# Kernel optimization log

Measured on AMD Instinct MI355X. Metric: run time of the kernel, lower is better.

Reference implementation:

```python
import jax, jax.numpy as jnp
import numpy as np

LN_EPS = 1e-3  # Keras LayerNormalization default epsilon


def setup_inputs() -> dict:
    key = jax.random.key(0)
    ks = jax.random.split(key, 6)
    B, H, W, C = 8, 64, 64, 256
    s = 1.0 / np.sqrt(C)
    return {
        "x": jax.random.normal(ks[0], (B, H, W, C), dtype=jnp.float32),
        "ln_gamma": jnp.ones((C,), jnp.float32),
        "ln_beta": jnp.zeros((C,), jnp.float32),
        "w_q": jax.random.normal(ks[1], (C, C), jnp.float32) * s,
        "b_q": jnp.zeros((C,), jnp.float32),
        "w_k": jax.random.normal(ks[2], (C, C), jnp.float32) * s,
        "b_k": jnp.zeros((C,), jnp.float32),
        "w_v": jax.random.normal(ks[3], (C, C), jnp.float32) * s,
        "b_v": jnp.zeros((C,), jnp.float32),
        "w_p": jax.random.normal(ks[4], (C, C), jnp.float32) * s,
        "b_p": jnp.zeros((C,), jnp.float32),
    }


def reference(x, ln_gamma, ln_beta, w_q, b_q, w_k, b_k, w_v, b_v, w_p, b_p):
    B, H, W, C = x.shape
    units = w_q.shape[1]
    scale = jnp.asarray(units, x.dtype) ** (-0.5)

    # LayerNormalization over the channel axis (Keras default eps=1e-3)
    mean = jnp.mean(x, axis=-1, keepdims=True)
    var = jnp.mean(jnp.square(x - mean), axis=-1, keepdims=True)
    xn = (x - mean) * jax.lax.rsqrt(var + LN_EPS) * ln_gamma + ln_beta

    xf = xn.reshape(B, H * W, C)  # flatten spatial grid to N tokens
    q = xf @ w_q + b_q
    k = xf @ w_k + b_k
    v = xf @ w_v + b_v

    # full quadratic attention over N = H*W tokens
    scores = jnp.einsum("bnc,bmc->bnm", q, k) * scale  # [B, N, N]
    attn = jax.nn.softmax(scores, axis=-1)
    out = jnp.einsum("bnm,bmc->bnc", attn, v)  # [B, N, units]
    proj = (out @ w_p + b_p).reshape(B, H, W, units)

    # NOTE: original code reassigns inputs = norm(inputs), so the residual
    # uses the normalized input, not the raw input.
    return xn + proj
```

## Files before the change

kernel.cpp:

```cpp
#include <hip/hip_runtime.h>
#include <cstdint>

#define NB    8
#define NSEQ  4096
#define CDIM  256
#define NTOK  (NB*NSEQ)

typedef _Float16 half8  __attribute__((ext_vector_type(8)));
typedef _Float16 half4v __attribute__((ext_vector_type(4)));
typedef float    f32x4  __attribute__((ext_vector_type(4)));
typedef float    f32x16 __attribute__((ext_vector_type(16)));
typedef uint32_t u32x4  __attribute__((ext_vector_type(4)));
typedef unsigned long u64x2 __attribute__((ext_vector_type(2)));

typedef unsigned int u32_g __attribute__((address_space(1)));
typedef unsigned int u32_l __attribute__((address_space(3)));

__device__ __forceinline__ void gload_lds16(const void* g, void* l) {
  __builtin_amdgcn_global_load_lds((u32_g*)(uintptr_t)g,
                                   (u32_l*)(uint32_t)(uintptr_t)l, 16, 0, 0);
}

__device__ __forceinline__ uint32_t pkrtz(float a, float b) {
  auto h = __builtin_amdgcn_cvt_pkrtz(a, b);
  return __builtin_bit_cast(uint32_t, h);
}
__device__ __forceinline__ uint8_t to_fp8(float v) {
  return (uint8_t)(__builtin_amdgcn_cvt_pk_fp8_f32(v, v, 0, false) & 0xff);
}
__device__ __forceinline__ float sx32f(float v) { return __shfl_xor(v, 32, 64); }
__device__ __forceinline__ uint32_t sx32u(uint32_t v) {
  return (uint32_t)__shfl_xor((int)v, 32, 64);
}

__global__ __launch_bounds__(256) void ln_kernel(
    const float* __restrict__ x, const float* __restrict__ gam,
    const float* __restrict__ bet, _Float16* __restrict__ xnh) {
  const int lane = threadIdx.x & 63;
  const size_t tok = (size_t)blockIdx.x * 4 + (threadIdx.x >> 6);
  const float4 v = ((const float4*)(x + tok * CDIM))[lane];
  float s  = v.x + v.y + v.z + v.w;
  float s2 = v.x*v.x + v.y*v.y + v.z*v.z + v.w*v.w;
  #pragma unroll
  for (int m = 1; m < 64; m <<= 1) {
    s  += __shfl_xor(s,  m, 64);
    s2 += __shfl_xor(s2, m, 64);
  }
  const float mean = s * (1.0f / CDIM);
  const float rstd = rsqrtf(s2 * (1.0f / CDIM) - mean * mean + 1e-3f);
  const float4 gv = ((const float4*)gam)[lane];
  const float4 bv = ((const float4*)bet)[lane];
  half4v h;
  h[0] = (_Float16)((v.x - mean) * rstd * gv.x + bv.x);
  h[1] = (_Float16)((v.y - mean) * rstd * gv.y + bv.y);
  h[2] = (_Float16)((v.z - mean) * rstd * gv.z + bv.z);
  h[3] = (_Float16)((v.w - mean) * rstd * gv.w + bv.w);
  ((half4v*)(xnh + tok * CDIM))[lane] = h;
}

__global__ __launch_bounds__(256, 2) void proj_kernel(
    const _Float16* __restrict__ inh,
    const float* __restrict__ wq_, const float* __restrict__ bq_,
    const float* __restrict__ wk_, const float* __restrict__ bk_,
    const float* __restrict__ wv_, const float* __restrict__ bv_,
    const float* __restrict__ wp_, const float* __restrict__ bp_,
    uint8_t* __restrict__ qg8, uint8_t* __restrict__ kg8,
    _Float16* __restrict__ vtg,
    const _Float16* __restrict__ residh, float* __restrict__ outf,
    int mode_base) {
  extern __shared__ char smem[];
  const int mode = mode_base + blockIdx.z;
  const float* wsel = (mode == 0) ? wq_ : (mode == 1) ? wk_ : (mode == 2) ? wv_ : wp_;
  const float* bsel = (mode == 0) ? bq_ : (mode == 1) ? bk_ : (mode == 2) ? bv_ : bp_;

  const int tid = threadIdx.x;
  const int lane = tid & 63;
  const int wid  = tid >> 6;
  const int g    = lane >> 4;
  const int lr   = lane & 15;
  const int jstrip = blockIdx.y;
  const size_t tok0 = (size_t)blockIdx.x * 512;

  char* wt   = smem;
  char* tile = smem + 32768;

  for (int i = 0; i < 64; ++i) {
    int idx = i * 256 + tid;
    int c = idx >> 6, j = idx & 63;
    float val = wsel[(size_t)c * CDIM + jstrip * 64 + j];
    *(_Float16*)(wt + j * 512 + ((((c >> 3) ^ (j & 7))) << 4) + ((c & 7) << 1)) =
        (_Float16)val;
  }
  float bjv[4];
  #pragma unroll
  for (int jc = 0; jc < 4; ++jc) bjv[jc] = bsel[jstrip * 64 + jc * 16 + lr];
  __syncthreads();

  for (int t = 0; t < 8; ++t) {
    const size_t trow0 = tok0 + t * 64;
    #pragma unroll
    for (int i = 0; i < 8; ++i) {
      int pbase = (i * 4 + wid) * 64;
      int p = pbase + lane;
      int row = p >> 5, sl = p & 31;
      gload_lds16(inh + (trow0 + row) * CDIM + (size_t)((sl ^ (row & 7)) * 8),
                  tile + pbase * 16);
    }
    __syncthreads();

    f32x4 acc[4] = {{0,0,0,0},{0,0,0,0},{0,0,0,0},{0,0,0,0}};
    #pragma unroll
    for (int kc = 0; kc < 8; ++kc) {
      half8 a = *(const half8*)(tile + (wid * 16 + lr) * 512 +
                                ((((kc << 2) | g) ^ (lr & 7)) << 4));
      #pragma unroll
      for (int jc = 0; jc < 4; ++jc) {
        half8 bf = *(const half8*)(wt + (jc * 16 + lr) * 512 +
                                   ((((kc << 2) | g) ^ (lr & 7)) << 4));
        acc[jc] = __builtin_amdgcn_mfma_f32_16x16x32_f16(a, bf, acc[jc], 0, 0, 0);
      }
    }

    if (mode == 3) {
      #pragma unroll
      for (int jc = 0; jc < 4; ++jc) {
        #pragma unroll
        for (int r = 0; r < 4; ++r) {
          size_t row = trow0 + wid * 16 + g * 4 + r;
          size_t off = row * CDIM + jstrip * 64 + jc * 16 + lr;
          outf[off] = acc[jc][r] + bjv[jc] + (float)residh[off];
        }
      }
    } else if (mode <= 1) {
      const float csc = (mode == 0) ? 1.44269504f : 1.0f;
      __syncthreads();
      uint8_t* ot8 = (uint8_t*)tile;
      #pragma unroll
      for (int jc = 0; jc < 4; ++jc) {
        #pragma unroll
        for (int r = 0; r < 4; ++r) {
          int row = wid * 16 + g * 4 + r;
          int pos = (jc >> 1) * 32 + (lr >> 3) * 16 + (jc & 1) * 8 + (lr & 7);
          ot8[row * 64 + pos] = to_fp8((acc[jc][r] + bjv[jc]) * csc);
        }
      }
      __syncthreads();
      uint8_t* dst8 = (mode == 0) ? qg8 : kg8;
      int row = tid >> 2, s = tid & 3;
      *(u32x4*)(dst8 + (trow0 + row) * 256 + jstrip * 64 + s * 16) =
          *(const u32x4*)(ot8 + row * 64 + s * 16);
    } else {
      __syncthreads();
      _Float16* ot = (_Float16*)tile;
      #pragma unroll
      for (int jc = 0; jc < 4; ++jc)
        #pragma unroll
        for (int r = 0; r < 4; ++r)
          ot[(wid * 16 + g * 4 + r) * 72 + jc * 16 + lr] =
              (_Float16)(acc[jc][r] + bjv[jc]);
      __syncthreads();
      #pragma unroll
      for (int it = 0; it < 2; ++it) {
        int s = it * 256 + tid;
        int j = s >> 3, ns = s & 7;
        half8 vv;
        #pragma unroll
        for (int e = 0; e < 8; ++e) vv[e] = ot[(ns * 8 + e) * 72 + j];
        size_t bb  = trow0 >> 12;
        size_t nin = (trow0 & 4095) + ns * 8;
        *(half8*)(vtg + ((size_t)bb * CDIM + jstrip * 64 + j) * NSEQ + nin) = vv;
      }
    }
    __syncthreads();
  }
}

#define ATTN_LDS 49152

__global__ __launch_bounds__(256)
__attribute__((amdgpu_waves_per_eu(2, 2)))
void attn_kernel(
    const uint8_t* __restrict__ qg8, const uint8_t* __restrict__ kg8,
    const _Float16* __restrict__ vtg, _Float16* __restrict__ po,
    float* __restrict__ mbuf, float* __restrict__ lbuf) {
  extern __shared__ char smem[];

  const int tid  = threadIdx.x;
  const int lane = tid & 63;
  const int wid  = tid >> 6;
  const int l31  = lane & 31;
  const int hi   = lane >> 5;
  const int bid  = blockIdx.x;
  const int b    = bid & 7;
  const int kvh  = (bid >> 3) & 1;
  const int n0   = (bid >> 4) * 128;
  const int kvbase = kvh * 2048;

  #pragma unroll
  for (int i = 0; i < 2; ++i) {
    int slot = i * 256 + wid * 64 + lane;
    int row = slot >> 4, s = slot & 15;
    gload_lds16(kg8 + ((size_t)(b * NSEQ + kvbase + row)) * 256 + ((s ^ (row & 7)) << 4),
                smem + slot * 16);
  }
  #pragma unroll
  for (int i = 0; i < 4; ++i) {
    int p = (i * 4 + wid) * 64 + lane;
    int d = p >> 2, vsl = p & 3;
    gload_lds16(vtg + ((size_t)(b * CDIM + d)) * NSEQ + kvbase + (vsl ^ (d & 3)) * 8,
                smem + 16384 + p * 16);
  }

  long qf8[16];
  {
    const uint8_t* qp8 = qg8 + ((size_t)(b * NSEQ + n0 + wid * 32 + l31)) * 256;
    #pragma unroll
    for (int p = 0; p < 8; ++p) {
      u64x2 qq = *(const u64x2*)(qp8 + (2 * p + hi) * 16);
      qf8[2 * p]     = (long)qq.x;
      qf8[2 * p + 1] = (long)qq.y;
    }
  }

  f32x16 o[8];
  #pragma unroll
  for (int dt = 0; dt < 8; ++dt)
    #pragma unroll
    for (int r = 0; r < 16; ++r) o[dt][r] = 0.0f;
  float mrun = -1e30f, lrun = 0.0f;

  __syncthreads();

  for (int t = 0; t < 64; ++t) {
    const int cur = t & 1;
    const char* kb = smem + cur * 8192;
    const char* vb = smem + 16384 + cur * 16384;

    if (t < 63) {
      const int kv0n = kvbase + (t + 1) * 32;
      char* kn = smem + (cur ^ 1) * 8192;
      char* vn = smem + 16384 + (cur ^ 1) * 16384;
      #pragma unroll
      for (int i = 0; i < 2; ++i) {
        int slot = i * 256 + wid * 64 + lane;
        int row = slot >> 4, s = slot & 15;
        gload_lds16(kg8 + ((size_t)(b * NSEQ + kv0n + row)) * 256 + ((s ^ (row & 7)) << 4),
                    kn + slot * 16);
      }
      #pragma unroll
      for (int i = 0; i < 4; ++i) {
        int p = (i * 4 + wid) * 64 + lane;
        int d = p >> 2, vsl = p & 3;
        gload_lds16(vtg + ((size_t)(b * CDIM + d)) * NSEQ + kv0n + (vsl ^ (d & 3)) * 8,
                    vn + p * 16);
      }
    }

    f32x16 sacc;
    #pragma unroll
    for (int r = 0; r < 16; ++r) sacc[r] = 0.0f;
    const char* krowp = kb + l31 * 256;
    #pragma unroll
    for (int p = 0; p < 8; ++p) {
      u64x2 kk = *(const u64x2*)(krowp + (((2 * p + hi) ^ (l31 & 7)) << 4));
      sacc = __builtin_amdgcn_mfma_f32_32x32x16_fp8_fp8((long)kk.x, qf8[2 * p],
                                                        sacc, 0, 0, 0);
      sacc = __builtin_amdgcn_mfma_f32_32x32x16_fp8_fp8((long)kk.y, qf8[2 * p + 1],
                                                        sacc, 0, 0, 0);
    }
    #pragma unroll
    for (int r = 0; r < 16; ++r) sacc[r] *= 0.0625f;

    float pm = sacc[0];
    #pragma unroll
    for (int r = 1; r < 16; ++r) pm = fmaxf(pm, sacc[r]);
    pm = fmaxf(pm, sx32f(pm));

    if (!__all(pm - mrun <= 8.0f)) {
      float mnew = fmaxf(mrun, pm);
      float al = exp2f(mrun - mnew);
      mrun = mnew;
      lrun *= al;
      #pragma unroll
      for (int r = 0; r < 16; ++r) {
        float ar = __shfl(al, (r & 3) + 8 * (r >> 2) + 4 * hi, 64);
        #pragma unroll
        for (int dt = 0; dt < 8; ++dt) o[dt][r] *= ar;
      }
    }

    float ls = 0.0f;
    #pragma unroll
    for (int r = 0; r < 16; ++r) { sacc[r] = exp2f(sacc[r] - mrun); ls += sacc[r]; }
    lrun += ls + sx32f(ls);

    half8 pa0, pa1;
    {
      uint32_t c0 = pkrtz(sacc[0], sacc[1]), c1 = pkrtz(sacc[2], sacc[3]);
      uint32_t c2 = pkrtz(sacc[4], sacc[5]), c3 = pkrtz(sacc[6], sacc[7]);
      uint32_t t0 = sx32u(c0), t1 = sx32u(c1), t2 = sx32u(c2), t3 = sx32u(c3);
      pa0 = __builtin_bit_cast(half8, (u32x4){
          hi ? t2 : c0, hi ? t3 : c1, hi ? c2 : t0, hi ? c3 : t1});
    }
    {
      uint32_t c0 = pkrtz(sacc[8], sacc[9]),  c1 = pkrtz(sacc[10], sacc[11]);
      uint32_t c2 = pkrtz(sacc[12], sacc[13]), c3 = pkrtz(sacc[14], sacc[15]);
      uint32_t t0 = sx32u(c0), t1 = sx32u(c1), t2 = sx32u(c2), t3 = sx32u(c3);
      pa1 = __builtin_bit_cast(half8, (u32x4){
          hi ? t2 : c0, hi ? t3 : c1, hi ? c2 : t0, hi ? c3 : t1});
    }

    #pragma unroll
    for (int dt = 0; dt < 8; ++dt) {
      const char* vrow = vb + (dt * 32 + l31) * 64;
      const int vx = (dt * 32 + l31) & 3;
      half8 vf0 = *(const half8*)(vrow + (((0 + hi) ^ vx) << 4));
      half8 vf1 = *(const half8*)(vrow + (((2 + hi) ^ vx) << 4));
      o[dt] = __builtin_amdgcn_mfma_f32_32x32x16_f16(pa0, vf0, o[dt], 0, 0, 0);
      o[dt] = __builtin_amdgcn_mfma_f32_32x32x16_f16(pa1, vf1, o[dt], 0, 0, 0);
    }

    __syncthreads();
  }

  const size_t tok0 = (size_t)b * NSEQ + n0 + wid * 32;
  if (lane < 32) {
    mbuf[(size_t)kvh * NTOK + tok0 + l31] = mrun;
    lbuf[(size_t)kvh * NTOK + tok0 + l31] = lrun;
  }
  #pragma unroll
  for (int r = 0; r < 16; ++r) {
    int q = (r & 3) + 8 * (r >> 2) + 4 * hi;
    _Float16* prow = po + ((size_t)kvh * NTOK + tok0 + q) * CDIM + l31;
    #pragma unroll
    for (int dt = 0; dt < 8; ++dt)
      prow[dt * 32] = (_Float16)o[dt][r];
  }
}

__global__ __launch_bounds__(256) void merge_kernel(
    const _Float16* __restrict__ po, const float* __restrict__ mbuf,
    const float* __restrict__ lbuf, _Float16* __restrict__ og) {
  const int lane = threadIdx.x & 63;
  const size_t tok = (size_t)blockIdx.x * 4 + (threadIdx.x >> 6);
  const float m0 = mbuf[tok], m1 = mbuf[NTOK + tok];
  const float l0 = lbuf[tok], l1 = lbuf[NTOK + tok];
  const float mm = fmaxf(m0, m1);
  const float a0 = exp2f(m0 - mm), a1 = exp2f(m1 - mm);
  const float rl = 1.0f / (l0 * a0 + l1 * a1);
  const half4v o0 = ((const half4v*)(po + tok * CDIM))[lane];
  const half4v o1 = ((const half4v*)(po + ((size_t)NTOK + tok) * CDIM))[lane];
  half4v out;
  #pragma unroll
  for (int j = 0; j < 4; ++j)
    out[j] = (_Float16)(((float)o0[j] * a0 + (float)o1[j] * a1) * rl);
  ((half4v*)(og + tok * CDIM))[lane] = out;
}

extern "C" void kernel_launch(void* const* d_in, const int* in_sizes, int n_in,
                              void* d_out, int out_size, void* d_ws, size_t ws_size,
                              hipStream_t stream) {
  const float* x   = (const float*)d_in[0];
  const float* gam = (const float*)d_in[1];
  const float* bet = (const float*)d_in[2];
  const float* wq  = (const float*)d_in[3];
  const float* bq  = (const float*)d_in[4];
  const float* wk  = (const float*)d_in[5];
  const float* bk  = (const float*)d_in[6];
  const float* wv  = (const float*)d_in[7];
  const float* bv  = (const float*)d_in[8];
  const float* wp  = (const float*)d_in[9];
  const float* bp  = (const float*)d_in[10];
  float* out = (float*)d_out;

  char* ws = (char*)d_ws;
  _Float16* po  = (_Float16*)ws;
  _Float16* xnh = (_Float16*)(ws + (32u << 20));
  uint8_t*  qh8 = (uint8_t*)(ws + (48u << 20));
  uint8_t*  kh8 = (uint8_t*)(ws + (56u << 20));
  _Float16* vth = (_Float16*)(ws + (64u << 20));
  _Float16* oh  = (_Float16*)(ws + (80u << 20));
  float*    mbf = (float*)(ws + (96u << 20));
  float*    lbf = (float*)(ws + (96u << 20) + (1u << 18));

  (void)hipFuncSetAttribute((const void*)proj_kernel,
                            hipFuncAttributeMaxDynamicSharedMemorySize, 65536);
  (void)hipFuncSetAttribute((const void*)attn_kernel,
                            hipFuncAttributeMaxDynamicSharedMemorySize, ATTN_LDS);

  ln_kernel<<<NTOK / 4, 256, 0, stream>>>(x, gam, bet, xnh);
  proj_kernel<<<dim3(64, 4, 3), 256, 65536, stream>>>(
      xnh, wq, bq, wk, bk, wv, bv, wp, bp, qh8, kh8, vth, xnh, out, 0);
  attn_kernel<<<512, 256, ATTN_LDS, stream>>>(qh8, kh8, vth, po, mbf, lbf);
  merge_kernel<<<NTOK / 4, 256, 0, stream>>>(po, mbf, lbf, oh);
  proj_kernel<<<dim3(64, 4, 1), 256, 65536, stream>>>(
      oh, wq, bq, wk, bk, wv, bv, wp, bp, qh8, kh8, vth, xnh, out, 3);
}
```

Measured before the change: 228.4 us.

## Switch PV matmul to FP8 with pre-swizzled FP8 V layout

Measured after the change: 193.2 us. -15.4%, faster.

```diff
diff --git a/kernel.cpp b/kernel.cpp
--- a/kernel.cpp
+++ b/kernel.cpp
@@ -21,12 +21,12 @@
                                    (u32_l*)(uint32_t)(uintptr_t)l, 16, 0, 0);
 }
 
-__device__ __forceinline__ uint32_t pkrtz(float a, float b) {
-  auto h = __builtin_amdgcn_cvt_pkrtz(a, b);
-  return __builtin_bit_cast(uint32_t, h);
-}
 __device__ __forceinline__ uint8_t to_fp8(float v) {
   return (uint8_t)(__builtin_amdgcn_cvt_pk_fp8_f32(v, v, 0, false) & 0xff);
+}
+__device__ __forceinline__ uint32_t pk4_fp8(float a, float b, float c, float d) {
+  uint32_t w = (uint32_t)__builtin_amdgcn_cvt_pk_fp8_f32(a, b, 0, false);
+  return (uint32_t)__builtin_amdgcn_cvt_pk_fp8_f32(c, d, (int)w, true);
 }
 __device__ __forceinline__ float sx32f(float v) { return __shfl_xor(v, 32, 64); }
 __device__ __forceinline__ uint32_t sx32u(uint32_t v) {
@@ -65,7 +65,7 @@
     const float* __restrict__ wv_, const float* __restrict__ bv_,
     const float* __restrict__ wp_, const float* __restrict__ bp_,
     uint8_t* __restrict__ qg8, uint8_t* __restrict__ kg8,
-    _Float16* __restrict__ vtg,
+    uint8_t* __restrict__ vt8,
     const _Float16* __restrict__ residh, float* __restrict__ outf,
     int mode_base) {
   extern __shared__ char smem[];
@@ -151,37 +151,38 @@
           *(const u32x4*)(ot8 + row * 64 + s * 16);
     } else {
       __syncthreads();
-      _Float16* ot = (_Float16*)tile;
-      #pragma unroll
-      for (int jc = 0; jc < 4; ++jc)
+      uint8_t* ot8 = (uint8_t*)tile;
+      #pragma unroll
+      for (int jc = 0; jc < 4; ++jc) {
         #pragma unroll
-        for (int r = 0; r < 4; ++r)
-          ot[(wid * 16 + g * 4 + r) * 72 + jc * 16 + lr] =
-              (_Float16)(acc[jc][r] + bjv[jc]);
+        for (int r = 0; r < 4; ++r) {
+          int tok64 = wid * 16 + g * 4 + r;
+          int kvblk = tok64 >> 5, kv = tok64 & 31;
+          int dl = jc * 16 + lr;
+          int sel = (kv >> 3) & 1;
+          int pos = (kv & 7) + ((kv >> 4) & 1) * 8;
+          int sloc = (dl >> 3) * 16 + sel * 8 + (dl & 7);
+          ot8[kvblk * 2048 + sloc * 16 + pos] = to_fp8(acc[jc][r] + bjv[jc]);
+        }
+      }
       __syncthreads();
-      #pragma unroll
-      for (int it = 0; it < 2; ++it) {
-        int s = it * 256 + tid;
-        int j = s >> 3, ns = s & 7;
-        half8 vv;
-        #pragma unroll
-        for (int e = 0; e < 8; ++e) vv[e] = ot[(ns * 8 + e) * 72 + j];
-        size_t bb  = trow0 >> 12;
-        size_t nin = (trow0 & 4095) + ns * 8;
-        *(half8*)(vtg + ((size_t)bb * CDIM + jstrip * 64 + j) * NSEQ + nin) = vv;
-      }
+      int kvblk = tid >> 7, sl = tid & 127;
+      size_t bb = trow0 >> 12;
+      size_t nblk = ((trow0 & 4095) >> 5) + kvblk;
+      *(u32x4*)(vt8 + ((bb * 128 + nblk) * 512 + jstrip * 128 + sl) * 16) =
+          *(const u32x4*)(ot8 + kvblk * 2048 + sl * 16);
     }
     __syncthreads();
   }
 }
 
-#define ATTN_LDS 49152
+#define ATTN_LDS 32768
 
 __global__ __launch_bounds__(256)
 __attribute__((amdgpu_waves_per_eu(2, 2)))
 void attn_kernel(
     const uint8_t* __restrict__ qg8, const uint8_t* __restrict__ kg8,
-    const _Float16* __restrict__ vtg, _Float16* __restrict__ po,
+    const uint8_t* __restrict__ vt8, _Float16* __restrict__ po,
     float* __restrict__ mbuf, float* __restrict__ lbuf) {
   extern __shared__ char smem[];
 
@@ -198,17 +199,12 @@
 
   #pragma unroll
   for (int i = 0; i < 2; ++i) {
-    int slot = i * 256 + wid * 64 + lane;
+    int slot = i * 256 + tid;
     int row = slot >> 4, s = slot & 15;
     gload_lds16(kg8 + ((size_t)(b * NSEQ + kvbase + row)) * 256 + ((s ^ (row & 7)) << 4),
                 smem + slot * 16);
-  }
-  #pragma unroll
-  for (int i = 0; i < 4; ++i) {
-    int p = (i * 4 + wid) * 64 + lane;
-    int d = p >> 2, vsl = p & 3;
-    gload_lds16(vtg + ((size_t)(b * CDIM + d)) * NSEQ + kvbase + (vsl ^ (d & 3)) * 8,
-                smem + 16384 + p * 16);
+    gload_lds16(vt8 + ((size_t)(b * 128 + kvh * 64) * 512 + slot) * 16,
+                smem + 16384 + slot * 16);
   }
 
   long qf8[16];
@@ -234,25 +230,20 @@
   for (int t = 0; t < 64; ++t) {
     const int cur = t & 1;
     const char* kb = smem + cur * 8192;
-    const char* vb = smem + 16384 + cur * 16384;
+    const char* vb = smem + 16384 + cur * 8192;
 
     if (t < 63) {
       const int kv0n = kvbase + (t + 1) * 32;
       char* kn = smem + (cur ^ 1) * 8192;
-      char* vn = smem + 16384 + (cur ^ 1) * 16384;
+      char* vn = smem + 16384 + (cur ^ 1) * 8192;
       #pragma unroll
       for (int i = 0; i < 2; ++i) {
-        int slot = i * 256 + wid * 64 + lane;
+        int slot = i * 256 + tid;
         int row = slot >> 4, s = slot & 15;
         gload_lds16(kg8 + ((size_t)(b * NSEQ + kv0n + row)) * 256 + ((s ^ (row & 7)) << 4),
                     kn + slot * 16);
-      }
-      #pragma unroll
-      for (int i = 0; i < 4; ++i) {
-        int p = (i * 4 + wid) * 64 + lane;
-        int d = p >> 2, vsl = p & 3;
-        gload_lds16(vtg + ((size_t)(b * CDIM + d)) * NSEQ + kv0n + (vsl ^ (d & 3)) * 8,
-                    vn + p * 16);
+        gload_lds16(vt8 + ((size_t)(b * 128 + kvh * 64 + t + 1) * 512 + slot) * 16,
+                    vn + slot * 16);
       }
     }
 
@@ -294,30 +285,20 @@
     for (int r = 0; r < 16; ++r) { sacc[r] = exp2f(sacc[r] - mrun); ls += sacc[r]; }
     lrun += ls + sx32f(ls);
 
-    half8 pa0, pa1;
-    {
-      uint32_t c0 = pkrtz(sacc[0], sacc[1]), c1 = pkrtz(sacc[2], sacc[3]);
-      uint32_t c2 = pkrtz(sacc[4], sacc[5]), c3 = pkrtz(sacc[6], sacc[7]);
-      uint32_t t0 = sx32u(c0), t1 = sx32u(c1), t2 = sx32u(c2), t3 = sx32u(c3);
-      pa0 = __builtin_bit_cast(half8, (u32x4){
-          hi ? t2 : c0, hi ? t3 : c1, hi ? c2 : t0, hi ? c3 : t1});
-    }
-    {
-      uint32_t c0 = pkrtz(sacc[8], sacc[9]),  c1 = pkrtz(sacc[10], sacc[11]);
-      uint32_t c2 = pkrtz(sacc[12], sacc[13]), c3 = pkrtz(sacc[14], sacc[15]);
-      uint32_t t0 = sx32u(c0), t1 = sx32u(c1), t2 = sx32u(c2), t3 = sx32u(c3);
-      pa1 = __builtin_bit_cast(half8, (u32x4){
-          hi ? t2 : c0, hi ? t3 : c1, hi ? c2 : t0, hi ? c3 : t1});
-    }
+    uint32_t w0 = pk4_fp8(sacc[0],  sacc[1],  sacc[2],  sacc[3]);
+    uint32_t w1 = pk4_fp8(sacc[4],  sacc[5],  sacc[6],  sacc[7]);
+    uint32_t w2 = pk4_fp8(sacc[8],  sacc[9],  sacc[10], sacc[11]);
+    uint32_t w3 = pk4_fp8(sacc[12], sacc[13], sacc[14], sacc[15]);
+    uint32_t t0 = sx32u(w0), t1 = sx32u(w1), t2 = sx32u(w2), t3 = sx32u(w3);
+    long pa0 = (long)(((uint64_t)(hi ? w1 : t0) << 32) | (uint32_t)(hi ? t1 : w0));
+    long pa1 = (long)(((uint64_t)(hi ? w3 : t2) << 32) | (uint32_t)(hi ? t3 : w2));
 
     #pragma unroll
     for (int dt = 0; dt < 8; ++dt) {
-      const char* vrow = vb + (dt * 32 + l31) * 64;
-      const int vx = (dt * 32 + l31) & 3;
-      half8 vf0 = *(const half8*)(vrow + (((0 + hi) ^ vx) << 4));
-      half8 vf1 = *(const half8*)(vrow + (((2 + hi) ^ vx) << 4));
-      o[dt] = __builtin_amdgcn_mfma_f32_32x32x16_f16(pa0, vf0, o[dt], 0, 0, 0);
-      o[dt] = __builtin_amdgcn_mfma_f32_32x32x16_f16(pa1, vf1, o[dt], 0, 0, 0);
+      const int dv = dt * 32 + l31;
+      u64x2 vv = *(const u64x2*)(vb + (dv >> 3) * 256 + hi * 128 + (dv & 7) * 16);
+      o[dt] = __builtin_amdgcn_mfma_f32_32x32x16_fp8_fp8(pa0, (long)vv.x, o[dt], 0, 0, 0);
+      o[dt] = __builtin_amdgcn_mfma_f32_32x32x16_fp8_fp8(pa1, (long)vv.y, o[dt], 0, 0, 0);
     }
 
     __syncthreads();
@@ -378,10 +359,10 @@
   _Float16* xnh = (_Float16*)(ws + (32u << 20));
   uint8_t*  qh8 = (uint8_t*)(ws + (48u << 20));
   uint8_t*  kh8 = (uint8_t*)(ws + (56u << 20));
-  _Float16* vth = (_Float16*)(ws + (64u << 20));
-  _Float16* oh  = (_Float16*)(ws + (80u << 20));
-  float*    mbf = (float*)(ws + (96u << 20));
-  float*    lbf = (float*)(ws + (96u << 20) + (1u << 18));
+  uint8_t*  vt8 = (uint8_t*)(ws + (64u << 20));
+  _Float16* oh  = (_Float16*)(ws + (72u << 20));
+  float*    mbf = (float*)(ws + (88u << 20));
+  float*    lbf = (float*)(ws + (88u << 20) + (1u << 18));
 
   (void)hipFuncSetAttribute((const void*)proj_kernel,
                             hipFuncAttributeMaxDynamicSharedMemorySize, 65536);
@@ -390,9 +371,9 @@
 
   ln_kernel<<<NTOK / 4, 256, 0, stream>>>(x, gam, bet, xnh);
   proj_kernel<<<dim3(64, 4, 3), 256, 65536, stream>>>(
-      xnh, wq, bq, wk, bk, wv, bv, wp, bp, qh8, kh8, vth, xnh, out, 0);
-  attn_kernel<<<512, 256, ATTN_LDS, stream>>>(qh8, kh8, vth, po, mbf, lbf);
+      xnh, wq, bq, wk, bk, wv, bv, wp, bp, qh8, kh8, vt8, xnh, out, 0);
+  attn_kernel<<<512, 256, ATTN_LDS, stream>>>(qh8, kh8, vt8, po, mbf, lbf);
   merge_kernel<<<NTOK / 4, 256, 0, stream>>>(po, mbf, lbf, oh);
   proj_kernel<<<dim3(64, 4, 1), 256, 65536, stream>>>(
-      oh, wq, bq, wk, bk, wv, bv, wp, bp, qh8, kh8, vth, xnh, out, 3);
-}
+      oh, wq, bq, wk, bk, wv, bv, wp, bp, qh8, kh8, vt8, xnh, out, 3);
+}
```
